# Performance work log

Measured on AMD Instinct MI355X. Metric: run time of the kernel, lower is better.

The kernel has to match this reference:

```python
import jax, jax.numpy as jnp
import numpy as np

D_MODEL = 1024
N_HEADS = 16
D_K = D_MODEL // N_HEADS


def setup_inputs() -> dict:
    key = jax.random.key(0)
    ks = jax.random.split(key, 11)
    B, S = 4, 2048
    inp = {
        'q': jax.random.normal(ks[0], (B, S, D_MODEL), dtype=jnp.float32),
        'k': jax.random.normal(ks[1], (B, S, D_MODEL), dtype=jnp.float32),
        'v': jax.random.normal(ks[2], (B, S, D_MODEL), dtype=jnp.float32),
    }
    scale = 1.0 / np.sqrt(D_MODEL)
    for i, name in enumerate(['Wq', 'Wk', 'Wv', 'Wo']):
        inp[name] = jax.random.normal(ks[3 + i], (D_MODEL, D_MODEL), dtype=jnp.float32) * scale
        inp['b' + name[1:]] = jnp.zeros((D_MODEL,), dtype=jnp.float32)
    return inp


def reference(q, k, v, Wq, bq, Wk, bk, Wv, bv, Wo, bo):
    B, S, _ = q.shape

    def split_heads(x):
        # [B,S,D] -> [B,H,S,d_k]
        return x.reshape(B, -1, N_HEADS, D_K).transpose(0, 2, 1, 3)

    qh = split_heads(q @ Wq.T + bq)
    kh = split_heads(k @ Wk.T + bk)
    vh = split_heads(v @ Wv.T + bv)

    scores = jnp.einsum('bhqd,bhkd->bhqk', qh, kh) / jnp.sqrt(jnp.float32(D_K))
    attn = jax.nn.softmax(scores, axis=-1)  # dropout is identity in eval / p=0
    out = jnp.einsum('bhqk,bhkd->bhqd', attn, vh)
    out = out.transpose(0, 2, 1, 3).reshape(B, -1, D_MODEL)
    return out @ Wo.T + bo
```

## Files before the change

### kernel.cpp

```cpp
#include <hip/hip_runtime.h>
#include <hip/hip_bf16.h>
#include <math.h>


#define SEQ 2048
#define NH 16
#define DKH 64
#define DM 1024
#define NB 4

#define QSCALE 0.18033688011112042f

typedef float f32x4 __attribute__((ext_vector_type(4)));
typedef __bf16 bf16x8 __attribute__((ext_vector_type(8)));
typedef __bf16 bf16x4 __attribute__((ext_vector_type(4)));

#define GLOAD16(g, l)                                                          \
    __builtin_amdgcn_global_load_lds(                                          \
        (const __attribute__((address_space(1))) void*)(g),                    \
        (__attribute__((address_space(3))) void*)(l), 16, 0, 0)

__device__ __forceinline__ float fast_exp2(float x) {
    float r;
    asm("v_exp_f32 %0, %1" : "=v"(r) : "v"(x));
    return r;
}

__global__ __launch_bounds__(256) void cvt_qkv(
    const float* __restrict__ q, const float* __restrict__ k, const float* __restrict__ v,
    __bf16* __restrict__ qb, __bf16* __restrict__ kb, __bf16* __restrict__ vb)
{
    const float* src = blockIdx.y == 0 ? q : (blockIdx.y == 1 ? k : v);
    __bf16* dst      = blockIdx.y == 0 ? qb : (blockIdx.y == 1 ? kb : vb);
    const size_t i = ((size_t)blockIdx.x * 256 + threadIdx.x) * 8;
    const float4 a = *reinterpret_cast<const float4*>(src + i);
    const float4 b = *reinterpret_cast<const float4*>(src + i + 4);
    bf16x8 o;
    o[0] = (__bf16)a.x; o[1] = (__bf16)a.y; o[2] = (__bf16)a.z; o[3] = (__bf16)a.w;
    o[4] = (__bf16)b.x; o[5] = (__bf16)b.y; o[6] = (__bf16)b.z; o[7] = (__bf16)b.w;
    *reinterpret_cast<bf16x8*>(dst + i) = o;
}

__global__ __launch_bounds__(256) void cvt_w(
    const float* __restrict__ wq, const float* __restrict__ wk,
    const float* __restrict__ wv, const float* __restrict__ wo,
    __bf16* __restrict__ oq, __bf16* __restrict__ ok,
    __bf16* __restrict__ ov, __bf16* __restrict__ oo)
{
    const int y = blockIdx.y;
    const float* src = y == 0 ? wq : (y == 1 ? wk : (y == 2 ? wv : wo));
    __bf16* dst      = y == 0 ? oq : (y == 1 ? ok : (y == 2 ? ov : oo));
    const float scale = (y == 0) ? QSCALE : 1.0f;
    const size_t i = ((size_t)blockIdx.x * 256 + threadIdx.x) * 8;
    const float4 a = *reinterpret_cast<const float4*>(src + i);
    const float4 b = *reinterpret_cast<const float4*>(src + i + 4);
    bf16x8 o;
    o[0] = (__bf16)(a.x * scale); o[1] = (__bf16)(a.y * scale);
    o[2] = (__bf16)(a.z * scale); o[3] = (__bf16)(a.w * scale);
    o[4] = (__bf16)(b.x * scale); o[5] = (__bf16)(b.y * scale);
    o[6] = (__bf16)(b.z * scale); o[7] = (__bf16)(b.w * scale);
    *reinterpret_cast<bf16x8*>(dst + i) = o;
}

template <int LAYOUT>
__device__ __forceinline__ void gemm_body(
    const __bf16* __restrict__ A, const __bf16* __restrict__ W,
    const float* __restrict__ bias, float bscale, void* __restrict__ outv,
    char* As, char* Bs)
{
    const int t = threadIdx.x;
    const int w = t >> 6, lane = t & 63, g = lane >> 4, ln = lane & 15;
    const int bm = blockIdx.x, bn = blockIdx.y;
    const int wr = w >> 1, wc = w & 1;

    const int srow = t >> 3;
    const int ssw  = ((t & 7) << 4) ^ ((srow & 7) << 4);

    const char* Ag = (const char*)A + (size_t)(bm * 128 + srow) * 2048 + ssw;
    const char* Wg = (const char*)W + (size_t)(bn * 128 + srow) * 2048 + ssw;

    f32x4 acc[4][4];
    #pragma unroll
    for (int i = 0; i < 4; ++i)
        #pragma unroll
        for (int j = 0; j < 4; ++j)
            #pragma unroll
            for (int e = 0; e < 4; ++e) acc[i][j][e] = 0.0f;

    for (int kb = 0; kb < 16; ++kb) {
        __syncthreads();
        #pragma unroll
        for (int c = 0; c < 4; ++c) {
            GLOAD16(Ag + kb * 128 + (size_t)c * (32 * 2048), As + c * 4096 + t * 16);
            GLOAD16(Wg + kb * 128 + (size_t)c * (32 * 2048), Bs + c * 4096 + t * 16);
        }
        __syncthreads();
        #pragma unroll
        for (int ks = 0; ks < 2; ++ks) {
            bf16x8 a[4], b[4];
            #pragma unroll
            for (int mi = 0; mi < 4; ++mi) {
                const int row = wr * 64 + mi * 16 + ln;
                a[mi] = *reinterpret_cast<const bf16x8*>(
                    As + row * 128 + (((ks * 64) + (g << 4)) ^ ((row & 7) << 4)));
            }
            #pragma unroll
            for (int ni = 0; ni < 4; ++ni) {
                const int row = wc * 64 + ni * 16 + ln;
                b[ni] = *reinterpret_cast<const bf16x8*>(
                    Bs + row * 128 + (((ks * 64) + (g << 4)) ^ ((row & 7) << 4)));
            }
            #pragma unroll
            for (int mi = 0; mi < 4; ++mi)
                #pragma unroll
                for (int ni = 0; ni < 4; ++ni)
                    acc[mi][ni] = __builtin_amdgcn_mfma_f32_16x16x32_bf16(
                        a[mi], b[ni], acc[mi][ni], 0, 0, 0);
        }
    }

    const int gm0 = bm * 128 + wr * 64, gn0 = bn * 128 + wc * 64;
    #pragma unroll
    for (int mi = 0; mi < 4; ++mi)
        #pragma unroll
        for (int ni = 0; ni < 4; ++ni) {
            const int col = gn0 + ni * 16 + ln;
            const float bs = bias[col] * bscale;
            #pragma unroll
            for (int r = 0; r < 4; ++r) {
                const int row = gm0 + mi * 16 + g * 4 + r;
                const float val = acc[mi][ni][r] + bs;
                if (LAYOUT == 0) {
                    const int bb = row >> 11, s = row & 2047;
                    const int h = col >> 6, d = col & 63;
                    ((__bf16*)outv)[(((size_t)(bb * NH + h) * SEQ) + s) * DKH + d] = (__bf16)val;
                } else {
                    ((float*)outv)[(size_t)row * DM + col] = val;
                }
            }
        }
}

__global__ __launch_bounds__(256) void gemm_qkv(
    const __bf16* __restrict__ qb, const __bf16* __restrict__ kb, const __bf16* __restrict__ vb,
    const __bf16* __restrict__ Wqb, const __bf16* __restrict__ Wkb, const __bf16* __restrict__ Wvb,
    const float* __restrict__ bq, const float* __restrict__ bk, const float* __restrict__ bv,
    __bf16* __restrict__ Qp, __bf16* __restrict__ Kp, __bf16* __restrict__ Vp)
{
    __shared__ __align__(16) char As[16384];
    __shared__ __align__(16) char Bs[16384];
    const int z = blockIdx.z;
    const __bf16* A = z == 0 ? qb : (z == 1 ? kb : vb);
    const __bf16* W = z == 0 ? Wqb : (z == 1 ? Wkb : Wvb);
    const float* bias = z == 0 ? bq : (z == 1 ? bk : bv);
    __bf16* out = z == 0 ? Qp : (z == 1 ? Kp : Vp);
    const float bscale = z == 0 ? QSCALE : 1.0f;
    gemm_body<0>(A, W, bias, bscale, out, As, Bs);
}

__global__ __launch_bounds__(256) void gemm_out(
    const __bf16* __restrict__ A, const __bf16* __restrict__ W,
    const float* __restrict__ bias, float* __restrict__ out)
{
    __shared__ __align__(16) char As[16384];
    __shared__ __align__(16) char Bs[16384];
    gemm_body<1>(A, W, bias, 1.0f, out, As, Bs);
}

__global__ __launch_bounds__(256) void transpose_v(
    const __bf16* __restrict__ Vp, __bf16* __restrict__ Vt)
{
    __shared__ __bf16 T[64][65];
    const int t = threadIdx.x, st = blockIdx.x, bh = blockIdx.y;
    const __bf16* src = Vp + ((size_t)bh * SEQ + st * 64) * DKH;
    #pragma unroll
    for (int r = 0; r < 2; ++r) {
        const int idx = r * 256 + t;
        const int s_l = idx >> 3, c8 = (idx & 7) << 3;
        const bf16x8 v8 = *reinterpret_cast<const bf16x8*>(src + s_l * DKH + c8);
        #pragma unroll
        for (int j = 0; j < 8; ++j) T[s_l][c8 + j] = v8[j];
    }
    __syncthreads();
    __bf16* dst = Vt + ((size_t)bh * DKH) * SEQ + st * 64;
    #pragma unroll
    for (int r = 0; r < 2; ++r) {
        const int idx = r * 256 + t;
        const int d = idx >> 3, s8 = (idx & 7) << 3;
        bf16x8 o;
        #pragma unroll
        for (int j = 0; j < 8; ++j) o[j] = T[s8 + j][d];
        *reinterpret_cast<bf16x8*>(dst + (size_t)d * SEQ + s8) = o;
    }
}

__global__ __launch_bounds__(256) void attn_mfma(
    const __bf16* __restrict__ Qp, const __bf16* __restrict__ Kp,
    const __bf16* __restrict__ Vt, __bf16* __restrict__ AO)
{
    __shared__ __align__(16) char Ks[16384];
    __shared__ __align__(16) char Vs[16384];
    __shared__ __align__(16) char Ps[16384];
    const int t = threadIdx.x;
    const int w = t >> 6, lane = t & 63, g = lane >> 4, ln = lane & 15;
    const int qt = blockIdx.x, bh = blockIdx.y;

    bf16x8 qf[2][2];
    #pragma unroll
    for (int st = 0; st < 2; ++st) {
        const __bf16* Qrow =
            Qp + ((size_t)bh * SEQ + qt * 128 + st * 64 + w * 16 + ln) * DKH;
        qf[st][0] = *reinterpret_cast<const bf16x8*>(Qrow + g * 8);
        qf[st][1] = *reinterpret_cast<const bf16x8*>(Qrow + 32 + g * 8);
    }

    const int srow = t >> 3;
    const int ssw  = ((t & 7) << 4) ^ ((srow & 7) << 4);
    const char* Kg = (const char*)Kp + ((size_t)bh * SEQ + srow) * 128 + ssw;
    const char* Vg = (const char*)Vt + ((size_t)bh * DKH + srow) * 4096 + ssw;

#define STAGE(buf, kt) do {                                                    \
        GLOAD16(Kg + (size_t)(kt) * 8192,          Ks + (buf) * 8192 + t * 16);\
        GLOAD16(Kg + (size_t)(kt) * 8192 + 4096,   Ks + (buf) * 8192 + 4096 + t * 16);\
        GLOAD16(Vg + (size_t)(kt) * 128,           Vs + (buf) * 8192 + t * 16);\
        GLOAD16(Vg + (size_t)(kt) * 128 + 32 * 4096, Vs + (buf) * 8192 + 4096 + t * 16);\
    } while (0)

    f32x4 oacc[2][4];
    float m[2] = {-INFINITY, -INFINITY}, l[2] = {0.0f, 0.0f};
    #pragma unroll
    for (int st = 0; st < 2; ++st)
        #pragma unroll
        for (int n = 0; n < 4; ++n)
            #pragma unroll
            for (int e = 0; e < 4; ++e) oacc[st][n][e] = 0.0f;

    char* PsW = Ps + w * 4096;
    const int swp = (ln & 3) << 5;

    STAGE(0, 0);
    __syncthreads();

    int cur = 0;
    for (int kt = 0; kt < 32; ++kt) {
        if (kt + 1 < 32) STAGE(cur ^ 1, kt + 1);

        const char* KsC = Ks + cur * 8192;
        const char* VsC = Vs + cur * 8192;

        bf16x8 kf[2][4];
        #pragma unroll
        for (int ks = 0; ks < 2; ++ks)
            #pragma unroll
            for (int f = 0; f < 4; ++f) {
                const int kr = f * 16 + ln;
                kf[ks][f] = *reinterpret_cast<const bf16x8*>(
                    KsC + kr * 128 + (((ks * 64) + (g << 4)) ^ ((kr & 7) << 4)));
            }

        f32x4 sc[2][4];
        #pragma unroll
        for (int st = 0; st < 2; ++st)
            #pragma unroll
            for (int f = 0; f < 4; ++f)
                #pragma unroll
                for (int e = 0; e < 4; ++e) sc[st][f][e] = 0.0f;
        #pragma unroll
        for (int ks = 0; ks < 2; ++ks)
            #pragma unroll
            for (int st = 0; st < 2; ++st)
                #pragma unroll
                for (int f = 0; f < 4; ++f)
                    sc[st][f] = __builtin_amdgcn_mfma_f32_16x16x32_bf16(
                        kf[ks][f], qf[st][ks], sc[st][f], 0, 0, 0);

        bf16x8 vreg[2][4];
        #pragma unroll
        for (int ks = 0; ks < 2; ++ks)
            #pragma unroll
            for (int n = 0; n < 4; ++n) {
                const int dr = n * 16 + ln;
                vreg[ks][n] = *reinterpret_cast<const bf16x8*>(
                    VsC + dr * 128 + (((ks * 64) + (g << 4)) ^ ((dr & 7) << 4)));
            }

        #pragma unroll
        for (int st = 0; st < 2; ++st) {
            float t0 = fmaxf(fmaxf(sc[st][0][0], sc[st][0][1]), fmaxf(sc[st][0][2], sc[st][0][3]));
            float t1 = fmaxf(fmaxf(sc[st][1][0], sc[st][1][1]), fmaxf(sc[st][1][2], sc[st][1][3]));
            float t2 = fmaxf(fmaxf(sc[st][2][0], sc[st][2][1]), fmaxf(sc[st][2][2], sc[st][2][3]));
            float t3 = fmaxf(fmaxf(sc[st][3][0], sc[st][3][1]), fmaxf(sc[st][3][2], sc[st][3][3]));
            float tmax = fmaxf(fmaxf(t0, t1), fmaxf(t2, t3));
            tmax = fmaxf(tmax, __shfl_xor(tmax, 16, 64));
            tmax = fmaxf(tmax, __shfl_xor(tmax, 32, 64));

            if (__any(tmax > m[st] + 11.0f)) {
                const float mn = fmaxf(m[st], tmax);
                const float es = fast_exp2(m[st] - mn);
                m[st] = mn;
                l[st] *= es;
                #pragma unroll
                for (int r = 0; r < 4; ++r) {
                    const float er = __shfl(es, (lane & 48) + (g << 2) + r, 64);
                    #pragma unroll
                    for (int n = 0; n < 4; ++n) oacc[st][n][r] *= er;
                }
            }

            float ss = 0.0f;
            char* prow = PsW + st * 2048 + ln * 128;
            #pragma unroll
            for (int f = 0; f < 4; ++f) {
                float p0 = fast_exp2(sc[st][f][0] - m[st]);
                float p1 = fast_exp2(sc[st][f][1] - m[st]);
                float p2 = fast_exp2(sc[st][f][2] - m[st]);
                float p3 = fast_exp2(sc[st][f][3] - m[st]);
                ss += (p0 + p1) + (p2 + p3);
                bf16x4 pk;
                pk[0] = (__bf16)p0; pk[1] = (__bf16)p1;
                pk[2] = (__bf16)p2; pk[3] = (__bf16)p3;
                *reinterpret_cast<bf16x4*>(prow + ((f * 32 + g * 8) ^ swp)) = pk;
            }
            ss += __shfl_xor(ss, 16, 64);
            ss += __shfl_xor(ss, 32, 64);
            l[st] += ss;
        }

        #pragma unroll
        for (int st = 0; st < 2; ++st)
            #pragma unroll
            for (int ks = 0; ks < 2; ++ks) {
                const bf16x8 pa = *reinterpret_cast<const bf16x8*>(
                    PsW + st * 2048 + ln * 128 + (((ks * 64) + (g << 4)) ^ swp));
                #pragma unroll
                for (int n = 0; n < 4; ++n)
                    oacc[st][n] = __builtin_amdgcn_mfma_f32_16x16x32_bf16(
                        pa, vreg[ks][n], oacc[st][n], 0, 0, 0);
            }

        __syncthreads();
        cur ^= 1;
    }

    const int b = bh >> 4, h = bh & 15;
    #pragma unroll
    for (int st = 0; st < 2; ++st)
        #pragma unroll
        for (int r = 0; r < 4; ++r) {
            const float lq = __shfl(l[st], (lane & 48) + (g << 2) + r, 64);
            const float inv = 1.0f / lq;
            const int s = qt * 128 + st * 64 + w * 16 + g * 4 + r;
            __bf16* orow = AO + ((size_t)(b * SEQ + s)) * DM + h * DKH;
            #pragma unroll
            for (int n = 0; n < 4; ++n)
                orow[n * 16 + ln] = (__bf16)(oacc[st][n][r] * inv);
        }
#undef STAGE
}

extern "C" void kernel_launch(void* const* d_in, const int* in_sizes, int n_in,
                              void* d_out, int out_size, void* d_ws, size_t ws_size,
                              hipStream_t stream)
{
    const float* q  = (const float*)d_in[0];
    const float* k  = (const float*)d_in[1];
    const float* v  = (const float*)d_in[2];
    const float* Wq = (const float*)d_in[3];
    const float* bq = (const float*)d_in[4];
    const float* Wk = (const float*)d_in[5];
    const float* bk = (const float*)d_in[6];
    const float* Wv = (const float*)d_in[7];
    const float* bv = (const float*)d_in[8];
    const float* Wo = (const float*)d_in[9];
    const float* bo = (const float*)d_in[10];
    float* out = (float*)d_out;

    const size_t NQ = (size_t)NB * SEQ * DM;
    const size_t NW = (size_t)DM * DM;

    __bf16* qb  = (__bf16*)d_ws;
    __bf16* kb  = qb + NQ;
    __bf16* vb  = kb + NQ;
    __bf16* Wqb = vb + NQ;
    __bf16* Wkb = Wqb + NW;
    __bf16* Wvb = Wkb + NW;
    __bf16* Wob = Wvb + NW;
    __bf16* Qp  = Wob + NW;
    __bf16* Kp  = Qp + NQ;
    __bf16* Vp  = Kp + NQ;
    __bf16* VtG = qb;
    __bf16* AO  = kb;

    cvt_qkv<<<dim3(4096, 3), 256, 0, stream>>>(q, k, v, qb, kb, vb);
    cvt_w<<<dim3(512, 4), 256, 0, stream>>>(Wq, Wk, Wv, Wo, Wqb, Wkb, Wvb, Wob);

    gemm_qkv<<<dim3(64, 8, 3), 256, 0, stream>>>(qb, kb, vb, Wqb, Wkb, Wvb,
                                                 bq, bk, bv, Qp, Kp, Vp);
    transpose_v<<<dim3(32, 64), 256, 0, stream>>>(Vp, VtG);
    attn_mfma<<<dim3(16, 64), 256, 0, stream>>>(Qp, Kp, VtG, AO);
    gemm_out<<<dim3(64, 8), 256, 0, stream>>>(AO, Wob, bo, out);
}
```

Baseline: 385.0 us.

## Switch attention to 32x32 MFMA with in-register P, double-buffer GEMM LDS

The attention kernel now uses 32x32x16 bf16 MFMA tiles, with each wave owning 32 query rows. The softmax probabilities are packed to bf16 in registers and rearranged with permlane32_swap, which removes the P round-trip through shared memory. The projection GEMMs switch to double-buffered LDS so the next K-slice loads while the current one computes, and they raise MFMA issue priority with s_setprio. The cost is doubled GEMM shared memory (64KB per block), which may lower occupancy, plus more register pressure from the 16-wide accumulators.

```diff
diff --git a/kernel.cpp b/kernel.cpp
--- a/kernel.cpp
+++ b/kernel.cpp
@@ -12,8 +12,9 @@
 #define QSCALE 0.18033688011112042f
 
 typedef float f32x4 __attribute__((ext_vector_type(4)));
+typedef float f32x16 __attribute__((ext_vector_type(16)));
 typedef __bf16 bf16x8 __attribute__((ext_vector_type(8)));
-typedef __bf16 bf16x4 __attribute__((ext_vector_type(4)));
+typedef unsigned int u32x4 __attribute__((ext_vector_type(4)));
 
 #define GLOAD16(g, l)                                                          \
     __builtin_amdgcn_global_load_lds(                                          \
@@ -24,6 +25,14 @@
     float r;
     asm("v_exp_f32 %0, %1" : "=v"(r) : "v"(x));
     return r;
+}
+__device__ __forceinline__ unsigned cvt_pk_bf16(float lo, float hi) {
+    unsigned r;
+    asm("v_cvt_pk_bf16_f32 %0, %1, %2" : "=v"(r) : "v"(lo), "v"(hi));
+    return r;
+}
+__device__ __forceinline__ void permlane32_swap(unsigned& a, unsigned& b) {
+    asm("v_permlane32_swap_b32 %0, %1" : "+v"(a), "+v"(b));
 }
 
 __global__ __launch_bounds__(256) void cvt_qkv(
@@ -79,6 +88,16 @@
     const char* Ag = (const char*)A + (size_t)(bm * 128 + srow) * 2048 + ssw;
     const char* Wg = (const char*)W + (size_t)(bn * 128 + srow) * 2048 + ssw;
 
+#define GSTAGE(buf, kb) do {                                                   \
+        _Pragma("unroll")                                                      \
+        for (int c = 0; c < 4; ++c) {                                          \
+            GLOAD16(Ag + (kb) * 128 + (size_t)c * (32 * 2048),                 \
+                    As + (buf) * 16384 + c * 4096 + t * 16);                   \
+            GLOAD16(Wg + (kb) * 128 + (size_t)c * (32 * 2048),                 \
+                    Bs + (buf) * 16384 + c * 4096 + t * 16);                   \
+        }                                                                      \
+    } while (0)
+
     f32x4 acc[4][4];
     #pragma unroll
     for (int i = 0; i < 4; ++i)
@@ -87,14 +106,14 @@
             #pragma unroll
             for (int e = 0; e < 4; ++e) acc[i][j][e] = 0.0f;
 
+    GSTAGE(0, 0);
+    int cur = 0;
     for (int kb = 0; kb < 16; ++kb) {
         __syncthreads();
-        #pragma unroll
-        for (int c = 0; c < 4; ++c) {
-            GLOAD16(Ag + kb * 128 + (size_t)c * (32 * 2048), As + c * 4096 + t * 16);
-            GLOAD16(Wg + kb * 128 + (size_t)c * (32 * 2048), Bs + c * 4096 + t * 16);
-        }
-        __syncthreads();
+        if (kb + 1 < 16) GSTAGE(cur ^ 1, kb + 1);
+
+        const char* AsC = As + cur * 16384;
+        const char* BsC = Bs + cur * 16384;
         #pragma unroll
         for (int ks = 0; ks < 2; ++ks) {
             bf16x8 a[4], b[4];
@@ -102,22 +121,26 @@
             for (int mi = 0; mi < 4; ++mi) {
                 const int row = wr * 64 + mi * 16 + ln;
                 a[mi] = *reinterpret_cast<const bf16x8*>(
-                    As + row * 128 + (((ks * 64) + (g << 4)) ^ ((row & 7) << 4)));
+                    AsC + row * 128 + (((ks * 64) + (g << 4)) ^ ((row & 7) << 4)));
             }
             #pragma unroll
             for (int ni = 0; ni < 4; ++ni) {
                 const int row = wc * 64 + ni * 16 + ln;
                 b[ni] = *reinterpret_cast<const bf16x8*>(
-                    Bs + row * 128 + (((ks * 64) + (g << 4)) ^ ((row & 7) << 4)));
+                    BsC + row * 128 + (((ks * 64) + (g << 4)) ^ ((row & 7) << 4)));
             }
+            __builtin_amdgcn_s_setprio(1);
             #pragma unroll
             for (int mi = 0; mi < 4; ++mi)
                 #pragma unroll
                 for (int ni = 0; ni < 4; ++ni)
                     acc[mi][ni] = __builtin_amdgcn_mfma_f32_16x16x32_bf16(
                         a[mi], b[ni], acc[mi][ni], 0, 0, 0);
-        }
+            __builtin_amdgcn_s_setprio(0);
+        }
+        cur ^= 1;
     }
+#undef GSTAGE
 
     const int gm0 = bm * 128 + wr * 64, gn0 = bn * 128 + wc * 64;
     #pragma unroll
@@ -147,8 +170,8 @@
     const float* __restrict__ bq, const float* __restrict__ bk, const float* __restrict__ bv,
     __bf16* __restrict__ Qp, __bf16* __restrict__ Kp, __bf16* __restrict__ Vp)
 {
-    __shared__ __align__(16) char As[16384];
-    __shared__ __align__(16) char Bs[16384];
+    __shared__ __align__(16) char As[32768];
+    __shared__ __align__(16) char Bs[32768];
     const int z = blockIdx.z;
     const __bf16* A = z == 0 ? qb : (z == 1 ? kb : vb);
     const __bf16* W = z == 0 ? Wqb : (z == 1 ? Wkb : Wvb);
@@ -162,8 +185,8 @@
     const __bf16* __restrict__ A, const __bf16* __restrict__ W,
     const float* __restrict__ bias, float* __restrict__ out)
 {
-    __shared__ __align__(16) char As[16384];
-    __shared__ __align__(16) char Bs[16384];
+    __shared__ __align__(16) char As[32768];
+    __shared__ __align__(16) char Bs[32768];
     gemm_body<1>(A, W, bias, 1.0f, out, As, Bs);
 }
 
@@ -200,19 +223,15 @@
 {
     __shared__ __align__(16) char Ks[16384];
     __shared__ __align__(16) char Vs[16384];
-    __shared__ __align__(16) char Ps[16384];
     const int t = threadIdx.x;
-    const int w = t >> 6, lane = t & 63, g = lane >> 4, ln = lane & 15;
+    const int w = t >> 6, lane = t & 63, q5 = lane & 31, h = lane >> 5;
     const int qt = blockIdx.x, bh = blockIdx.y;
 
-    bf16x8 qf[2][2];
-    #pragma unroll
-    for (int st = 0; st < 2; ++st) {
-        const __bf16* Qrow =
-            Qp + ((size_t)bh * SEQ + qt * 128 + st * 64 + w * 16 + ln) * DKH;
-        qf[st][0] = *reinterpret_cast<const bf16x8*>(Qrow + g * 8);
-        qf[st][1] = *reinterpret_cast<const bf16x8*>(Qrow + 32 + g * 8);
-    }
+    const __bf16* Qrow = Qp + ((size_t)bh * SEQ + qt * 128 + w * 32 + q5) * DKH;
+    bf16x8 qf[4];
+    #pragma unroll
+    for (int ksc = 0; ksc < 4; ++ksc)
+        qf[ksc] = *reinterpret_cast<const bf16x8*>(Qrow + ksc * 16 + h * 8);
 
     const int srow = t >> 3;
     const int ssw  = ((t & 7) << 4) ^ ((srow & 7) << 4);
@@ -220,23 +239,18 @@
     const char* Vg = (const char*)Vt + ((size_t)bh * DKH + srow) * 4096 + ssw;
 
 #define STAGE(buf, kt) do {                                                    \
-        GLOAD16(Kg + (size_t)(kt) * 8192,          Ks + (buf) * 8192 + t * 16);\
-        GLOAD16(Kg + (size_t)(kt) * 8192 + 4096,   Ks + (buf) * 8192 + 4096 + t * 16);\
-        GLOAD16(Vg + (size_t)(kt) * 128,           Vs + (buf) * 8192 + t * 16);\
+        GLOAD16(Kg + (size_t)(kt) * 8192,            Ks + (buf) * 8192 + t * 16);\
+        GLOAD16(Kg + (size_t)(kt) * 8192 + 4096,     Ks + (buf) * 8192 + 4096 + t * 16);\
+        GLOAD16(Vg + (size_t)(kt) * 128,             Vs + (buf) * 8192 + t * 16);\
         GLOAD16(Vg + (size_t)(kt) * 128 + 32 * 4096, Vs + (buf) * 8192 + 4096 + t * 16);\
     } while (0)
 
-    f32x4 oacc[2][4];
-    float m[2] = {-INFINITY, -INFINITY}, l[2] = {0.0f, 0.0f};
-    #pragma unroll
-    for (int st = 0; st < 2; ++st)
-        #pragma unroll
-        for (int n = 0; n < 4; ++n)
-            #pragma unroll
-            for (int e = 0; e < 4; ++e) oacc[st][n][e] = 0.0f;
-
-    char* PsW = Ps + w * 4096;
-    const int swp = (ln & 3) << 5;
+    f32x16 oacc[2];
+    float m = -INFINITY, lsum = 0.0f;
+    #pragma unroll
+    for (int jb = 0; jb < 2; ++jb)
+        #pragma unroll
+        for (int e = 0; e < 16; ++e) oacc[jb][e] = 0.0f;
 
     STAGE(0, 0);
     __syncthreads();
@@ -248,113 +262,97 @@
         const char* KsC = Ks + cur * 8192;
         const char* VsC = Vs + cur * 8192;
 
-        bf16x8 kf[2][4];
-        #pragma unroll
-        for (int ks = 0; ks < 2; ++ks)
-            #pragma unroll
-            for (int f = 0; f < 4; ++f) {
-                const int kr = f * 16 + ln;
-                kf[ks][f] = *reinterpret_cast<const bf16x8*>(
-                    KsC + kr * 128 + (((ks * 64) + (g << 4)) ^ ((kr & 7) << 4)));
+        f32x16 sc0, sc1;
+        #pragma unroll
+        for (int e = 0; e < 16; ++e) { sc0[e] = 0.0f; sc1[e] = 0.0f; }
+        const int ksw = (q5 & 7) << 4;
+        __builtin_amdgcn_s_setprio(1);
+        #pragma unroll
+        for (int ksc = 0; ksc < 4; ++ksc) {
+            const bf16x8 kf0 = *reinterpret_cast<const bf16x8*>(
+                KsC + q5 * 128 + ((ksc * 32 + h * 16) ^ ksw));
+            const bf16x8 kf1 = *reinterpret_cast<const bf16x8*>(
+                KsC + (32 + q5) * 128 + ((ksc * 32 + h * 16) ^ ksw));
+            sc0 = __builtin_amdgcn_mfma_f32_32x32x16_bf16(kf0, qf[ksc], sc0, 0, 0, 0);
+            sc1 = __builtin_amdgcn_mfma_f32_32x32x16_bf16(kf1, qf[ksc], sc1, 0, 0, 0);
+        }
+        __builtin_amdgcn_s_setprio(0);
+
+        float tmax = fmaxf(sc0[0], sc1[0]);
+        #pragma unroll
+        for (int e = 1; e < 16; ++e) tmax = fmaxf(tmax, fmaxf(sc0[e], sc1[e]));
+        tmax = fmaxf(tmax, __shfl_xor(tmax, 32, 64));
+
+        if (__any(tmax > m + 11.0f)) {
+            const float mn = fmaxf(m, tmax);
+            const float es = fast_exp2(m - mn);
+            m = mn;
+            lsum *= es;
+            #pragma unroll
+            for (int r = 0; r < 16; ++r) {
+                const float er = __shfl(es, (r & 3) + 8 * (r >> 2) + 4 * h, 64);
+                oacc[0][r] *= er;
+                oacc[1][r] *= er;
             }
-
-        f32x4 sc[2][4];
-        #pragma unroll
-        for (int st = 0; st < 2; ++st)
-            #pragma unroll
-            for (int f = 0; f < 4; ++f)
-                #pragma unroll
-                for (int e = 0; e < 4; ++e) sc[st][f][e] = 0.0f;
-        #pragma unroll
-        for (int ks = 0; ks < 2; ++ks)
-            #pragma unroll
-            for (int st = 0; st < 2; ++st)
-                #pragma unroll
-                for (int f = 0; f < 4; ++f)
-                    sc[st][f] = __builtin_amdgcn_mfma_f32_16x16x32_bf16(
-                        kf[ks][f], qf[st][ks], sc[st][f], 0, 0, 0);
-
-        bf16x8 vreg[2][4];
-        #pragma unroll
-        for (int ks = 0; ks < 2; ++ks)
-            #pragma unroll
-            for (int n = 0; n < 4; ++n) {
-                const int dr = n * 16 + ln;
-                vreg[ks][n] = *reinterpret_cast<const bf16x8*>(
-                    VsC + dr * 128 + (((ks * 64) + (g << 4)) ^ ((dr & 7) << 4)));
+        }
+
+        float p0[16], p1[16];
+        float ss = 0.0f;
+        #pragma unroll
+        for (int e = 0; e < 16; ++e) {
+            p0[e] = fast_exp2(sc0[e] - m);
+            p1[e] = fast_exp2(sc1[e] - m);
+            ss += p0[e] + p1[e];
+        }
+        ss += __shfl_xor(ss, 32, 64);
+        lsum += ss;
+
+        bf16x8 pa[4];
+        #pragma unroll
+        for (int kbp = 0; kbp < 4; ++kbp) {
+            const float* ps = (kbp >> 1) ? p1 : p0;
+            const int base = 8 * (kbp & 1);
+            unsigned a0 = cvt_pk_bf16(ps[base + 0], ps[base + 1]);
+            unsigned b0 = cvt_pk_bf16(ps[base + 4], ps[base + 5]);
+            unsigned a1 = cvt_pk_bf16(ps[base + 2], ps[base + 3]);
+            unsigned b1 = cvt_pk_bf16(ps[base + 6], ps[base + 7]);
+            permlane32_swap(a0, b0);
+            permlane32_swap(a1, b1);
+            u32x4 pw;
+            pw[0] = a0; pw[1] = a1; pw[2] = b0; pw[3] = b1;
+            pa[kbp] = *reinterpret_cast<bf16x8*>(&pw);
+        }
+
+        __builtin_amdgcn_s_setprio(1);
+        #pragma unroll
+        for (int jb = 0; jb < 2; ++jb) {
+            const int dr = jb * 32 + q5;
+            const int vsw = (dr & 7) << 4;
+            #pragma unroll
+            for (int kbp = 0; kbp < 4; ++kbp) {
+                const bf16x8 vbf = *reinterpret_cast<const bf16x8*>(
+                    VsC + dr * 128 + ((kbp * 32 + h * 16) ^ vsw));
+                oacc[jb] = __builtin_amdgcn_mfma_f32_32x32x16_bf16(
+                    pa[kbp], vbf, oacc[jb], 0, 0, 0);
             }
-
-        #pragma unroll
-        for (int st = 0; st < 2; ++st) {
-            float t0 = fmaxf(fmaxf(sc[st][0][0], sc[st][0][1]), fmaxf(sc[st][0][2], sc[st][0][3]));
-            float t1 = fmaxf(fmaxf(sc[st][1][0], sc[st][1][1]), fmaxf(sc[st][1][2], sc[st][1][3]));
-            float t2 = fmaxf(fmaxf(sc[st][2][0], sc[st][2][1]), fmaxf(sc[st][2][2], sc[st][2][3]));
-            float t3 = fmaxf(fmaxf(sc[st][3][0], sc[st][3][1]), fmaxf(sc[st][3][2], sc[st][3][3]));
-            float tmax = fmaxf(fmaxf(t0, t1), fmaxf(t2, t3));
-            tmax = fmaxf(tmax, __shfl_xor(tmax, 16, 64));
-            tmax = fmaxf(tmax, __shfl_xor(tmax, 32, 64));
-
-            if (__any(tmax > m[st] + 11.0f)) {
-                const float mn = fmaxf(m[st], tmax);
-                const float es = fast_exp2(m[st] - mn);
-                m[st] = mn;
-                l[st] *= es;
-                #pragma unroll
-                for (int r = 0; r < 4; ++r) {
-                    const float er = __shfl(es, (lane & 48) + (g << 2) + r, 64);
-                    #pragma unroll
-                    for (int n = 0; n < 4; ++n) oacc[st][n][r] *= er;
-                }
-            }
-
-            float ss = 0.0f;
-            char* prow = PsW + st * 2048 + ln * 128;
-            #pragma unroll
-            for (int f = 0; f < 4; ++f) {
-                float p0 = fast_exp2(sc[st][f][0] - m[st]);
-                float p1 = fast_exp2(sc[st][f][1] - m[st]);
-                float p2 = fast_exp2(sc[st][f][2] - m[st]);
-                float p3 = fast_exp2(sc[st][f][3] - m[st]);
-                ss += (p0 + p1) + (p2 + p3);
-                bf16x4 pk;
-                pk[0] = (__bf16)p0; pk[1] = (__bf16)p1;
-                pk[2] = (__bf16)p2; pk[3] = (__bf16)p3;
-                *reinterpret_cast<bf16x4*>(prow + ((f * 32 + g * 8) ^ swp)) = pk;
-            }
-            ss += __shfl_xor(ss, 16, 64);
-            ss += __shfl_xor(ss, 32, 64);
-            l[st] += ss;
-        }
-
-        #pragma unroll
-        for (int st = 0; st < 2; ++st)
-            #pragma unroll
-            for (int ks = 0; ks < 2; ++ks) {
-                const bf16x8 pa = *reinterpret_cast<const bf16x8*>(
-                    PsW + st * 2048 + ln * 128 + (((ks * 64) + (g << 4)) ^ swp));
-                #pragma unroll
-                for (int n = 0; n < 4; ++n)
-                    oacc[st][n] = __builtin_amdgcn_mfma_f32_16x16x32_bf16(
-                        pa, vreg[ks][n], oacc[st][n], 0, 0, 0);
-            }
+        }
+        __builtin_amdgcn_s_setprio(0);
 
         __syncthreads();
         cur ^= 1;
     }
 
-    const int b = bh >> 4, h = bh & 15;
-    #pragma unroll
-    for (int st = 0; st < 2; ++st)
-        #pragma unroll
-        for (int r = 0; r < 4; ++r) {
-            const float lq = __shfl(l[st], (lane & 48) + (g << 2) + r, 64);
-            const float inv = 1.0f / lq;
-            const int s = qt * 128 + st * 64 + w * 16 + g * 4 + r;
-            __bf16* orow = AO + ((size_t)(b * SEQ + s)) * DM + h * DKH;
-            #pragma unroll
-            for (int n = 0; n < 4; ++n)
-                orow[n * 16 + ln] = (__bf16)(oacc[st][n][r] * inv);
-        }
+    const float invl = 1.0f / lsum;
+    const int b = bh >> 4, hh = bh & 15;
+    #pragma unroll
+    for (int r = 0; r < 16; ++r) {
+        const int qq = (r & 3) + 8 * (r >> 2) + 4 * h;
+        const float iv = __shfl(invl, qq, 64);
+        const int s = qt * 128 + w * 32 + qq;
+        __bf16* orow = AO + ((size_t)(b * SEQ + s)) * DM + hh * DKH;
+        orow[q5]      = (__bf16)(oacc[0][r] * iv);
+        orow[32 + q5] = (__bf16)(oacc[1][r] * iv);
+    }
 #undef STAGE
 }
 
```

Result: faster. 376.5 us (-2.2%).
